# Optimization experiments

Measured on AMD Instinct MI355X. Metric: run time of the kernel, lower is better.

The kernel has to match this reference:

```python
import jax, jax.numpy as jnp
import numpy as np

N = 1536          # num nodes
E = 49152         # num edges (avg degree 32)
D_IN = 32         # in_channels_node
D_EA = 2          # in_channels_edge_attr
D_ET = 2          # in_channels_edge_type
EMB = 32          # edge_attr_emb = edge_type_emb = node_emb = out_channels
HEADS = 3
SLOPE = 0.2


def leaky(x):
    return jax.nn.leaky_relu(x, negative_slope=SLOPE)


def setup_inputs() -> dict:
    key = jax.random.key(0)
    ks = jax.random.split(key, 12)
    node_f = jax.random.normal(ks[0], (N, D_IN), dtype=jnp.float32)
    edge_index = jax.random.randint(ks[1], (2, E), 0, N, dtype=jnp.int32)
    edge_attr = jax.random.normal(ks[2], (E, D_EA), dtype=jnp.float32)
    edge_type = jax.random.uniform(ks[3], (E, D_ET), dtype=jnp.float32)
    veh_node_mask = jax.random.bernoulli(ks[4], 0.7, (N,))
    ped_node_mask = jnp.logical_not(veh_node_mask)
    s = 0.1
    W_veh = jax.random.normal(ks[5], (EMB, D_IN), dtype=jnp.float32) * s
    W_ped = jax.random.normal(ks[6], (EMB, D_IN), dtype=jnp.float32) * s
    W_ea = jax.random.normal(ks[7], (EMB, D_EA), dtype=jnp.float32) * s
    W_et = jax.random.normal(ks[8], (EMB, D_ET), dtype=jnp.float32) * s
    # attention_nn: Linear(edge_attr_emb + edge_type_emb + 2*node_emb -> heads)
    W_att = jax.random.normal(ks[9], (HEADS, 2 * EMB + 2 * EMB), dtype=jnp.float32) * s
    # node_update_emb: Linear(edge_attr_emb + node_emb -> out_channels)
    W_upd = jax.random.normal(ks[10], (EMB, 2 * EMB), dtype=jnp.float32) * s
    return dict(node_f=node_f, edge_attr=edge_attr, edge_type=edge_type,
                W_veh=W_veh, W_ped=W_ped, W_ea=W_ea, W_et=W_et,
                W_att=W_att, W_upd=W_upd,
                edge_index=edge_index, veh_node_mask=veh_node_mask,
                ped_node_mask=ped_node_mask)


def reference(node_f, edge_attr, edge_type, W_veh, W_ped, W_ea, W_et,
              W_att, W_upd, edge_index, veh_node_mask, ped_node_mask):
    n = node_f.shape[0]
    src, dst = edge_index[0], edge_index[1]

    # edge embeddings [E, 32] each
    emb_ea = leaky(edge_attr @ W_ea.T)
    emb_et = leaky(edge_type.astype(node_f.dtype) @ W_et.T)
    edge_f = jnp.concatenate([emb_ea, emb_et], axis=-1)        # [E, 64]

    # densify (sparse_coo_tensor -> to_dense sums duplicate indices)
    dense_edge = jnp.zeros((n, n, 2 * EMB), node_f.dtype).at[src, dst].add(edge_f)
    dense_ea = jnp.zeros((n, n, EMB), node_f.dtype).at[src, dst].add(emb_ea)
    adj = jnp.zeros((n, n), node_f.dtype).at[src, dst].add(1.0)

    # type-specific node embedding (ped assignment last, matching torch overwrite order)
    node_emb = jnp.where(veh_node_mask[:, None], node_f @ W_veh.T, 0.0)
    node_emb = jnp.where(ped_node_mask[:, None], node_f @ W_ped.T, node_emb)
    node_emb = leaky(node_emb)                                  # [N, 32]

    # attention scores: split the linear over the concatenated [tar | edge | nbr] features
    W_tar, W_edge, W_nbr = W_att[:, :EMB], W_att[:, EMB:3 * EMB], W_att[:, 3 * EMB:]
    scores = leaky((node_emb @ W_tar.T)[:, None, :]
                   + jnp.einsum('ijc,hc->ijh', dense_edge, W_edge)
                   + (node_emb @ W_nbr.T)[None, :, :])          # [N, N, H]

    scores = jnp.where(adj[:, :, None] == 0.0, jnp.float32(-10000.0), scores)
    attn = jax.nn.softmax(scores, axis=1)                       # softmax over neighbors

    # node update features: Linear over [edge_attr_emb | nbr_emb]; identical across heads
    Wu_e, Wu_n = W_upd[:, :EMB], W_upd[:, EMB:]
    upd = leaky(jnp.einsum('ijc,oc->ijo', dense_ea, Wu_e)
                + (node_emb @ Wu_n.T)[None, :, :])              # [N, N, 32]

    # weighted aggregation over neighbors, then concat heads
    next_node_f = jnp.einsum('ijh,ijo->iho', attn, upd)         # [N, H, 32]
    return next_node_f.reshape(n, HEADS * EMB)
```

## Files before the change

### kernel.cpp

```cpp
#include <hip/hip_runtime.h>
#include <stdint.h>

#define NN 1536
#define EE 49152
#define EMB 32
#define HEADS 3
#define SLOPE 0.2f
#define MAXP 1536
#define CHUNK 64

__device__ __forceinline__ float lrelu(float x){ return x >= 0.f ? x : SLOPE*x; }

__device__ int detect_mask_layout(const unsigned char* p){
  const int* pi = (const int*)p;
  bool ok = true;
  for (int k=0;k<64 && ok;k++){ int v = pi[k]; ok = (v==0 || v==1); }
  if (ok) return 0;
  ok = true;
  for (int k=0;k<256 && ok;k++){ ok = (p[k] <= 1); }
  if (ok) return 1;
  return 2;
}
__device__ bool mask_at(const unsigned char* p, int layout, int i){
  if (layout==0) return ((const int*)p)[i] != 0;
  if (layout==1) return p[i] != 0;
  return ((const float*)p)[i] != 0.f;
}

__global__ __launch_bounds__(256) void k_prep(
    const float* __restrict__ node_f,
    const float* __restrict__ W_veh, const float* __restrict__ W_ped,
    const float* __restrict__ W_att, const float* __restrict__ W_upd,
    const int* __restrict__ ei, const unsigned char* __restrict__ veh_mask,
    int* __restrict__ M, int* __restrict__ nxt,
    float* __restrict__ tar, float* __restrict__ nbr, float* __restrict__ nb)
{
  const int t = threadIdx.x;
  const int b = blockIdx.x;

  if (b < EE/256){
    const int e = b*256 + t;
    const int s = ei[e], d = ei[EE + e];
    nxt[e] = atomicExch(&M[s*NN + d], e);
    return;
  }

  __shared__ float sWvehT[EMB*33], sWpedT[EMB*33], sWunT[EMB*33];
  __shared__ float sWt[HEADS*EMB], sWn[HEADS*EMB];
  __shared__ float sF[8*EMB], sEmb[8*EMB];
  __shared__ int layout_s;
  const int i0 = (b - EE/256)*8;
  if (t == 0) layout_s = detect_mask_layout(veh_mask);
  for (int idx=t; idx<EMB*EMB; idx+=256){
    const int mm = idx>>5, kk = idx&31;
    sWvehT[mm*33+kk] = W_veh[idx];
    sWpedT[mm*33+kk] = W_ped[idx];
    sWunT[mm*33+kk]  = W_upd[mm*64 + EMB + kk];
  }
  if (t < HEADS*EMB){
    const int h = t>>5, c = t&31;
    sWt[t] = W_att[h*128 + c];
    sWn[t] = W_att[h*128 + 96 + c];
  }
  sF[t] = node_f[(size_t)i0*EMB + t];
  __syncthreads();

  const int li = t >> 5, m = t & 31;
  const int i = i0 + li;
  const bool veh = mask_at(veh_mask, layout_s, i);
  const float* WT = veh ? sWvehT : sWpedT;
  float a = 0.f;
  #pragma unroll
  for (int k=0;k<EMB;k++) a += sF[li*EMB+k] * WT[m*33+k];
  sEmb[li*EMB+m] = lrelu(a);
  __syncthreads();

  float bb = 0.f;
  #pragma unroll
  for (int k=0;k<EMB;k++) bb += sEmb[li*EMB+k] * sWunT[m*33+k];
  nb[(size_t)i*EMB + m] = bb;
  if (m < 3){
    float v = 0.f;
    #pragma unroll
    for (int k=0;k<EMB;k++) v += sEmb[li*EMB+k] * sWt[m*EMB+k];
    tar[i*4+m] = v;
  } else if (m < 6){
    const int h = m-3;
    float v = 0.f;
    #pragma unroll
    for (int k=0;k<EMB;k++) v += sEmb[li*EMB+k] * sWn[h*EMB+k];
    nbr[i*4+h] = v;
  }
}

__global__ __launch_bounds__(256) void k_rows(
    const int* __restrict__ M, const int* __restrict__ nxt,
    const float* __restrict__ edge_attr, const float* __restrict__ edge_type,
    const float* __restrict__ W_ea, const float* __restrict__ W_et,
    const float* __restrict__ W_att, const float* __restrict__ W_upd,
    const float* __restrict__ tar, const float* __restrict__ nbr,
    const float* __restrict__ nb, float* __restrict__ out)
{
  const int r = blockIdx.x;
  const int t = threadIdx.x;

  __shared__ int   pd[MAXP], pe[MAXP];
  __shared__ int   npair;
  __shared__ float sWea[EMB*2], sWet[EMB*2], sWedge[HEADS*64], sWueT[EMB*33];
  __shared__ float sA[CHUNK*33], sT[CHUNK*33];
  __shared__ float u_c[CHUNK*EMB];
  __shared__ float sc[192], p_c[192];
  __shared__ float m_run[3], l_run[3], alpha_s[3];

  if (t == 0) npair = 0;
  if (t < 3){ m_run[t] = -1e30f; l_run[t] = 0.f; }
  if (t < EMB*2){ sWea[t] = W_ea[t]; sWet[t] = W_et[t]; }
  if (t < HEADS*64) sWedge[t] = W_att[(t>>6)*128 + EMB + (t&63)];
  for (int idx=t; idx<EMB*EMB; idx+=256){
    const int o = idx>>5, k = idx&31;
    sWueT[o*33+k] = W_upd[o*64 + k];
  }
  __syncthreads();

  for (int j=t; j<NN; j+=256){
    const int v = M[(size_t)r*NN + j];
    if (v >= 0){
      const int idx = atomicAdd(&npair, 1);
      pd[idx] = j; pe[idx] = v;
    }
  }
  __syncthreads();
  const int Np = npair;

  if (Np == 0){
    __shared__ float fb[EMB];
    if (t < EMB) fb[t] = 0.f;
    __syncthreads();
    for (int idx=t; idx<NN*EMB; idx+=256)
      atomicAdd(&fb[idx&31], lrelu(nb[idx]));
    __syncthreads();
    if (t < 96) out[(size_t)r*96 + t] = fb[t&31] * (1.0f/NN);
    return;
  }

  float acc = 0.f;
  const int li = t >> 5, m = t & 31;
  const float wa0 = sWea[m*2], wa1 = sWea[m*2+1];
  const float wt0 = sWet[m*2], wt1 = sWet[m*2+1];

  for (int c0 = 0; c0 < Np; c0 += CHUNK){
    const int Cc = min(CHUNK, Np - c0);

    for (int q = li; q < Cc; q += 8){
      float am = 0.f, tm = 0.f;
      int e = pe[c0+q];
      while (e >= 0){
        const float2 ea = ((const float2*)edge_attr)[e];
        const float2 et = ((const float2*)edge_type)[e];
        am += lrelu(ea.x*wa0 + ea.y*wa1);
        tm += lrelu(et.x*wt0 + et.y*wt1);
        e = nxt[e];
      }
      sA[q*33+m] = am;
      sT[q*33+m] = tm;
    }
    __syncthreads();

    if (t < 192){
      const int h = t>>6, q = t&63;
      if (q < Cc){
        float se = 0.f;
        #pragma unroll
        for (int k=0;k<EMB;k++)
          se += sWedge[h*64+k]*sA[q*33+k] + sWedge[h*64+EMB+k]*sT[q*33+k];
        sc[t] = lrelu(tar[r*4+h] + se + nbr[pd[c0+q]*4+h]);
      }
    }
    for (int idx=t; idx<Cc*EMB; idx+=256){
      const int q = idx>>5, o = idx&31;
      float v = 0.f;
      #pragma unroll
      for (int k=0;k<EMB;k++) v += sWueT[o*33+k]*sA[q*33+k];
      u_c[idx] = lrelu(v + nb[(size_t)pd[c0+q]*EMB + o]);
    }
    __syncthreads();

    if (t < 3){
      float mn = m_run[t];
      for (int q=0;q<Cc;q++) mn = fmaxf(mn, sc[t*64+q]);
      alpha_s[t] = __expf(m_run[t] - mn);
      m_run[t] = mn;
    }
    __syncthreads();

    if (t < 192){
      const int h = t>>6, q = t&63;
      float p = (q < Cc) ? __expf(sc[t] - m_run[h]) : 0.f;
      p_c[t] = p;
      float sum = p;
      for (int d=32; d; d>>=1) sum += __shfl_xor(sum, d, 64);
      if ((t&63) == 0) l_run[h] = l_run[h]*alpha_s[h] + sum;
    }
    __syncthreads();

    if (t < 96){
      const int h = t>>5, o = t&31;
      float a2 = 0.f;
      for (int q=0;q<Cc;q++) a2 += p_c[h*64+q]*u_c[q*32+o];
      acc = acc*alpha_s[h] + a2;
    }
  }

  if (t < 96) out[(size_t)r*96 + t] = acc / l_run[t>>5];
}

extern "C" void kernel_launch(void* const* d_in, const int* in_sizes, int n_in,
                              void* d_out, int out_size, void* d_ws, size_t ws_size,
                              hipStream_t stream)
{
  (void)in_sizes; (void)n_in; (void)out_size; (void)ws_size;
  const float* node_f    = (const float*)d_in[0];
  const float* edge_attr = (const float*)d_in[1];
  const float* edge_type = (const float*)d_in[2];
  const float* W_veh     = (const float*)d_in[3];
  const float* W_ped     = (const float*)d_in[4];
  const float* W_ea      = (const float*)d_in[5];
  const float* W_et      = (const float*)d_in[6];
  const float* W_att     = (const float*)d_in[7];
  const float* W_upd     = (const float*)d_in[8];
  const int*   ei        = (const int*)d_in[9];
  const unsigned char* veh_mask = (const unsigned char*)d_in[10];
  float* out = (float*)d_out;

  char* ws = (char*)d_ws;
  const size_t oM   = 0;
  const size_t oNxt = oM   + (size_t)NN*NN*4;
  const size_t oTar = oNxt + (size_t)EE*4;
  const size_t oNbr = oTar + (size_t)NN*4*4;
  const size_t oNb  = oNbr + (size_t)NN*4*4;

  int*   M    = (int*)  (ws + oM);
  int*   nxt  = (int*)  (ws + oNxt);
  float* tar  = (float*)(ws + oTar);
  float* nbr  = (float*)(ws + oNbr);
  float* nb   = (float*)(ws + oNb);

  hipMemsetAsync(ws + oM, 0xFF, (size_t)NN*NN*4, stream);

  k_prep<<<EE/256 + NN/8, 256, 0, stream>>>(node_f, W_veh, W_ped, W_att, W_upd,
                                            ei, veh_mask, M, nxt, tar, nbr, nb);
  k_rows<<<NN, 256, 0, stream>>>(M, nxt, edge_attr, edge_type,
                                 W_ea, W_et, W_att, W_upd, tar, nbr, nb, out);
}
```

Before: 127.7 us.

## Replace dense adjacency map with per-source edge buckets and precomputed per-edge projections

Drops the N×N int map, along with its 9 MB memset and the full row scans, in favour of per-source-node bucket lists with a capacity of 256 built by atomics. Per-edge attention and update projections are computed once in the prep kernel and stored, so k_rows only groups duplicate destinations and sums the precomputed values. Each row block now runs a single-pass softmax instead of the chunked online version. Rows with more than CAP edges would be silently truncated, and duplicate detection is quadratic in row length.

```diff
diff --git a/kernel.cpp b/kernel.cpp
--- a/kernel.cpp
+++ b/kernel.cpp
@@ -6,8 +6,7 @@
 #define EMB 32
 #define HEADS 3
 #define SLOPE 0.2f
-#define MAXP 1536
-#define CHUNK 64
+#define CAP 256
 
 __device__ __forceinline__ float lrelu(float x){ return x >= 0.f ? x : SLOPE*x; }
 
@@ -29,19 +28,53 @@
 
 __global__ __launch_bounds__(256) void k_prep(
     const float* __restrict__ node_f,
+    const float* __restrict__ edge_attr, const float* __restrict__ edge_type,
     const float* __restrict__ W_veh, const float* __restrict__ W_ped,
+    const float* __restrict__ W_ea,  const float* __restrict__ W_et,
     const float* __restrict__ W_att, const float* __restrict__ W_upd,
     const int* __restrict__ ei, const unsigned char* __restrict__ veh_mask,
-    int* __restrict__ M, int* __restrict__ nxt,
+    int* __restrict__ cnt, int* __restrict__ bucket,
+    float* __restrict__ se_e, float* __restrict__ eau_e,
     float* __restrict__ tar, float* __restrict__ nbr, float* __restrict__ nb)
 {
   const int t = threadIdx.x;
   const int b = blockIdx.x;
 
-  if (b < EE/256){
-    const int e = b*256 + t;
-    const int s = ei[e], d = ei[EE + e];
-    nxt[e] = atomicExch(&M[s*NN + d], e);
+  if (b < EE/8){
+    __shared__ float sWea[64], sWet[64], sWedge[HEADS*64], sWueT[EMB*33];
+    __shared__ float sA[8*33], sT[8*33];
+    if (t < 64){ sWea[t] = W_ea[t]; sWet[t] = W_et[t]; }
+    if (t < HEADS*64) sWedge[t] = W_att[(t>>6)*128 + EMB + (t&63)];
+    for (int idx=t; idx<EMB*EMB; idx+=256){
+      const int o = idx>>5, k = idx&31;
+      sWueT[o*33+k] = W_upd[o*64 + k];
+    }
+    __syncthreads();
+
+    const int li = t >> 5, m = t & 31;
+    const int e = b*8 + li;
+    const float2 ea = ((const float2*)edge_attr)[e];
+    const float2 et = ((const float2*)edge_type)[e];
+    sA[li*33+m] = lrelu(ea.x*sWea[m*2] + ea.y*sWea[m*2+1]);
+    sT[li*33+m] = lrelu(et.x*sWet[m*2] + et.y*sWet[m*2+1]);
+    __syncthreads();
+
+    float v = 0.f;
+    #pragma unroll
+    for (int k=0;k<EMB;k++) v += sWueT[m*33+k] * sA[li*33+k];
+    eau_e[(size_t)e*EMB + m] = v;
+    if (m < HEADS){
+      float u = 0.f;
+      #pragma unroll
+      for (int k=0;k<EMB;k++)
+        u += sWedge[m*64+k]*sA[li*33+k] + sWedge[m*64+EMB+k]*sT[li*33+k];
+      se_e[(size_t)e*4 + m] = u;
+    }
+    if (m == 0){
+      const int s = ei[e];
+      const int idx = atomicAdd(&cnt[s], 1);
+      if (idx < CAP) bucket[(size_t)s*CAP + idx] = e;
+    }
     return;
   }
 
@@ -49,7 +82,7 @@
   __shared__ float sWt[HEADS*EMB], sWn[HEADS*EMB];
   __shared__ float sF[8*EMB], sEmb[8*EMB];
   __shared__ int layout_s;
-  const int i0 = (b - EE/256)*8;
+  const int i0 = (b - EE/8)*8;
   if (t == 0) layout_s = detect_mask_layout(veh_mask);
   for (int idx=t; idx<EMB*EMB; idx+=256){
     const int mm = idx>>5, kk = idx&31;
@@ -94,124 +127,106 @@
 }
 
 __global__ __launch_bounds__(256) void k_rows(
-    const int* __restrict__ M, const int* __restrict__ nxt,
-    const float* __restrict__ edge_attr, const float* __restrict__ edge_type,
-    const float* __restrict__ W_ea, const float* __restrict__ W_et,
-    const float* __restrict__ W_att, const float* __restrict__ W_upd,
+    const int* __restrict__ cnt, const int* __restrict__ bucket,
+    const int* __restrict__ ei,
+    const float* __restrict__ se_e, const float* __restrict__ eau_e,
     const float* __restrict__ tar, const float* __restrict__ nbr,
     const float* __restrict__ nb, float* __restrict__ out)
 {
   const int r = blockIdx.x;
   const int t = threadIdx.x;
-
-  __shared__ int   pd[MAXP], pe[MAXP];
-  __shared__ int   npair;
-  __shared__ float sWea[EMB*2], sWet[EMB*2], sWedge[HEADS*64], sWueT[EMB*33];
-  __shared__ float sA[CHUNK*33], sT[CHUNK*33];
-  __shared__ float u_c[CHUNK*EMB];
-  __shared__ float sc[192], p_c[192];
-  __shared__ float m_run[3], l_run[3], alpha_s[3];
-
-  if (t == 0) npair = 0;
-  if (t < 3){ m_run[t] = -1e30f; l_run[t] = 0.f; }
-  if (t < EMB*2){ sWea[t] = W_ea[t]; sWet[t] = W_et[t]; }
-  if (t < HEADS*64) sWedge[t] = W_att[(t>>6)*128 + EMB + (t&63)];
-  for (int idx=t; idx<EMB*EMB; idx+=256){
-    const int o = idx>>5, k = idx&31;
-    sWueT[o*33+k] = W_upd[o*64 + k];
-  }
-  __syncthreads();
-
-  for (int j=t; j<NN; j+=256){
-    const int v = M[(size_t)r*NN + j];
-    if (v >= 0){
-      const int idx = atomicAdd(&npair, 1);
-      pd[idx] = j; pe[idx] = v;
-    }
-  }
-  __syncthreads();
-  const int Np = npair;
-
-  if (Np == 0){
+  const int li = t >> 5, m = t & 31;
+
+  __shared__ int   le[CAP], ld[CAP], slotof[CAP], slotidx[CAP], cdst[CAP];
+  __shared__ float eau_sum[CAP*33];
+  __shared__ float se_sum[CAP*4];
+  __shared__ float sc[3*CAP], pp[3*CAP];
+  __shared__ float bmax[3], bden[3];
+  __shared__ int np_s;
+
+  if (t == 0) np_s = 0;
+  const int K = min(cnt[r], CAP);
+
+  if (K == 0){
     __shared__ float fb[EMB];
     if (t < EMB) fb[t] = 0.f;
     __syncthreads();
-    for (int idx=t; idx<NN*EMB; idx+=256)
-      atomicAdd(&fb[idx&31], lrelu(nb[idx]));
+    for (int idx=t; idx<NN*EMB; idx+=256) atomicAdd(&fb[idx&31], lrelu(nb[idx]));
     __syncthreads();
     if (t < 96) out[(size_t)r*96 + t] = fb[t&31] * (1.0f/NN);
     return;
   }
 
-  float acc = 0.f;
-  const int li = t >> 5, m = t & 31;
-  const float wa0 = sWea[m*2], wa1 = sWea[m*2+1];
-  const float wt0 = sWet[m*2], wt1 = sWet[m*2+1];
-
-  for (int c0 = 0; c0 < Np; c0 += CHUNK){
-    const int Cc = min(CHUNK, Np - c0);
-
-    for (int q = li; q < Cc; q += 8){
-      float am = 0.f, tm = 0.f;
-      int e = pe[c0+q];
-      while (e >= 0){
-        const float2 ea = ((const float2*)edge_attr)[e];
-        const float2 et = ((const float2*)edge_type)[e];
-        am += lrelu(ea.x*wa0 + ea.y*wa1);
-        tm += lrelu(et.x*wt0 + et.y*wt1);
-        e = nxt[e];
-      }
-      sA[q*33+m] = am;
-      sT[q*33+m] = tm;
-    }
-    __syncthreads();
-
-    if (t < 192){
-      const int h = t>>6, q = t&63;
-      if (q < Cc){
-        float se = 0.f;
-        #pragma unroll
-        for (int k=0;k<EMB;k++)
-          se += sWedge[h*64+k]*sA[q*33+k] + sWedge[h*64+EMB+k]*sT[q*33+k];
-        sc[t] = lrelu(tar[r*4+h] + se + nbr[pd[c0+q]*4+h]);
-      }
-    }
-    for (int idx=t; idx<Cc*EMB; idx+=256){
-      const int q = idx>>5, o = idx&31;
-      float v = 0.f;
-      #pragma unroll
-      for (int k=0;k<EMB;k++) v += sWueT[o*33+k]*sA[q*33+k];
-      u_c[idx] = lrelu(v + nb[(size_t)pd[c0+q]*EMB + o]);
-    }
-    __syncthreads();
-
-    if (t < 3){
-      float mn = m_run[t];
-      for (int q=0;q<Cc;q++) mn = fmaxf(mn, sc[t*64+q]);
-      alpha_s[t] = __expf(m_run[t] - mn);
-      m_run[t] = mn;
-    }
-    __syncthreads();
-
-    if (t < 192){
-      const int h = t>>6, q = t&63;
-      float p = (q < Cc) ? __expf(sc[t] - m_run[h]) : 0.f;
-      p_c[t] = p;
-      float sum = p;
-      for (int d=32; d; d>>=1) sum += __shfl_xor(sum, d, 64);
-      if ((t&63) == 0) l_run[h] = l_run[h]*alpha_s[h] + sum;
-    }
-    __syncthreads();
-
-    if (t < 96){
-      const int h = t>>5, o = t&31;
-      float a2 = 0.f;
-      for (int q=0;q<Cc;q++) a2 += p_c[h*64+q]*u_c[q*32+o];
-      acc = acc*alpha_s[h] + a2;
-    }
-  }
-
-  if (t < 96) out[(size_t)r*96 + t] = acc / l_run[t>>5];
+  for (int i=t; i<K; i+=256) le[i] = bucket[(size_t)r*CAP + i];
+  __syncthreads();
+  for (int i=t; i<K; i+=256) ld[i] = ei[EE + le[i]];
+  __syncthreads();
+
+  for (int i=t; i<K; i+=256){
+    const int d = ld[i];
+    bool canon = true;
+    for (int j=0;j<i;j++) if (ld[j]==d){ canon = false; break; }
+    if (canon){
+      const int s2 = atomicAdd(&np_s, 1);
+      slotidx[i] = s2;
+      cdst[s2] = d;
+    }
+  }
+  __syncthreads();
+  const int Kc = np_s;
+  for (int i=t; i<K; i+=256){
+    const int d = ld[i];
+    int c = i;
+    for (int j=0;j<i;j++) if (ld[j]==d){ c = j; break; }
+    slotof[i] = slotidx[c];
+  }
+  for (int idx=t; idx<Kc*33; idx+=256) eau_sum[idx] = 0.f;
+  for (int idx=t; idx<Kc*4;  idx+=256) se_sum[idx]  = 0.f;
+  __syncthreads();
+
+  for (int base=0; base<K; base+=8){
+    const int q = base + li;
+    if (q < K){
+      const int sl = slotof[q], e = le[q];
+      atomicAdd(&eau_sum[sl*33 + m], eau_e[(size_t)e*EMB + m]);
+      if (m < 3) atomicAdd(&se_sum[sl*4 + m], se_e[(size_t)e*4 + m]);
+    }
+  }
+  __syncthreads();
+
+  for (int idx=t; idx<3*CAP; idx+=256){
+    const int h = idx >> 8, q = idx & (CAP-1);
+    if (q < Kc)
+      sc[idx] = lrelu(tar[r*4+h] + se_sum[q*4+h] + nbr[cdst[q]*4+h]);
+  }
+  __syncthreads();
+  if (t < 3){
+    float mn = -1e30f;
+    for (int q=0;q<Kc;q++) mn = fmaxf(mn, sc[t*CAP+q]);
+    bmax[t] = mn;
+  }
+  __syncthreads();
+  for (int idx=t; idx<3*CAP; idx+=256){
+    const int h = idx >> 8, q = idx & (CAP-1);
+    pp[idx] = (q < Kc) ? __expf(sc[idx] - bmax[h]) : 0.f;
+  }
+  __syncthreads();
+  if (t < 3){
+    float s = 0.f;
+    for (int q=0;q<Kc;q++) s += pp[t*CAP+q];
+    bden[t] = s;
+  }
+  __syncthreads();
+
+  if (t < 96){
+    const int h = t >> 5, o = t & 31;
+    float acc = 0.f;
+    for (int q=0;q<Kc;q++){
+      const float u = lrelu(eau_sum[q*33+o] + nb[(size_t)cdst[q]*EMB + o]);
+      acc += pp[h*CAP+q] * u;
+    }
+    out[(size_t)r*96 + t] = acc / bden[h];
+  }
 }
 
 extern "C" void kernel_launch(void* const* d_in, const int* in_sizes, int n_in,
@@ -233,22 +248,27 @@
   float* out = (float*)d_out;
 
   char* ws = (char*)d_ws;
-  const size_t oM   = 0;
-  const size_t oNxt = oM   + (size_t)NN*NN*4;
-  const size_t oTar = oNxt + (size_t)EE*4;
+  const size_t oCnt = 0;
+  const size_t oBkt = oCnt + (size_t)NN*4;
+  const size_t oTar = oBkt + (size_t)NN*CAP*4;
   const size_t oNbr = oTar + (size_t)NN*4*4;
   const size_t oNb  = oNbr + (size_t)NN*4*4;
-
-  int*   M    = (int*)  (ws + oM);
-  int*   nxt  = (int*)  (ws + oNxt);
-  float* tar  = (float*)(ws + oTar);
-  float* nbr  = (float*)(ws + oNbr);
-  float* nb   = (float*)(ws + oNb);
-
-  hipMemsetAsync(ws + oM, 0xFF, (size_t)NN*NN*4, stream);
-
-  k_prep<<<EE/256 + NN/8, 256, 0, stream>>>(node_f, W_veh, W_ped, W_att, W_upd,
-                                            ei, veh_mask, M, nxt, tar, nbr, nb);
-  k_rows<<<NN, 256, 0, stream>>>(M, nxt, edge_attr, edge_type,
-                                 W_ea, W_et, W_att, W_upd, tar, nbr, nb, out);
-}
+  const size_t oSe  = oNb  + (size_t)NN*EMB*4;
+  const size_t oEau = oSe  + (size_t)EE*4*4;
+
+  int*   cnt    = (int*)  (ws + oCnt);
+  int*   bucket = (int*)  (ws + oBkt);
+  float* tar    = (float*)(ws + oTar);
+  float* nbr    = (float*)(ws + oNbr);
+  float* nb     = (float*)(ws + oNb);
+  float* se_e   = (float*)(ws + oSe);
+  float* eau_e  = (float*)(ws + oEau);
+
+  hipMemsetAsync(ws + oCnt, 0, (size_t)NN*4, stream);
+
+  k_prep<<<EE/8 + NN/8, 256, 0, stream>>>(node_f, edge_attr, edge_type,
+                                          W_veh, W_ped, W_ea, W_et, W_att, W_upd,
+                                          ei, veh_mask, cnt, bucket, se_e, eau_e,
+                                          tar, nbr, nb);
+  k_rows<<<NN, 256, 0, stream>>>(cnt, bucket, ei, se_e, eau_e, tar, nbr, nb, out);
+}
```

Result: slower. 148.5 us (+16.3%).
